# Kernel tuning notes

Measured on AMD Instinct MI355X. Metric: run time of the kernel, lower is better.

Reference implementation:

```python
import jax, jax.numpy as jnp
import numpy as np

B, N, ND = 4096, 28, 3        # batch, nodes (2 hands x 14 joints), xyz
ED, DD = 512, 256             # encoder dim, decoder dim
H, DH = 8, 64                 # heads, dim_head (inner = 512)
EDEPTH, DDEPTH = 2, 1
EMLP, DMLP = 4 * ED, 4 * DD
NM = 14                       # num_masked = int(0.5 * 28)


def _ln(x, s, b):
    m = jnp.mean(x, -1, keepdims=True)
    v = jnp.var(x, -1, keepdims=True)
    return (x - m) * jax.lax.rsqrt(v + 1e-5) * s + b


def _transformer(x, a, ln1_s, ln1_b, Wqkv, Wo, bo, ln2_s, ln2_b, W1, b1, W2, b2):
    # pre-norm transformer; adjacency a [b,n,n] enters as an additive attention bias
    b, n, _ = x.shape
    scale = DH ** -0.5
    for i in range(ln1_s.shape[0]):
        h = _ln(x, ln1_s[i], ln1_b[i])
        q, k, v = jnp.split(h @ Wqkv[i], 3, axis=-1)
        q = q.reshape(b, n, H, DH).transpose(0, 2, 1, 3)
        k = k.reshape(b, n, H, DH).transpose(0, 2, 1, 3)
        v = v.reshape(b, n, H, DH).transpose(0, 2, 1, 3)
        dots = jnp.einsum('bhid,bhjd->bhij', q, k) * scale + a[:, None]
        attn = jax.nn.softmax(dots, axis=-1)
        o = jnp.einsum('bhij,bhjd->bhid', attn, v).transpose(0, 2, 1, 3).reshape(b, n, H * DH)
        x = x + o @ Wo[i] + bo[i]
        h2 = _ln(x, ln2_s[i], ln2_b[i])
        x = x + jax.nn.gelu(h2 @ W1[i] + b1[i]) @ W2[i] + b2[i]
    return x


def setup_inputs() -> dict:
    key = jax.random.key(0)
    ks = iter(jax.random.split(key, 40))
    nrm = lambda shp, s=0.02: jax.random.normal(next(ks), shp, dtype=jnp.float32) * s
    x = jax.random.normal(next(ks), (B, N, ND), dtype=jnp.float32)
    a = jax.random.uniform(next(ks), (B, N, N), dtype=jnp.float32)
    perm = jnp.argsort(jax.random.uniform(next(ks), (B, N)), axis=-1).astype(jnp.int32)
    masked_indices, unmasked_indices = perm[:, :NM], perm[:, NM:]
    inp = dict(x=x, a=a, masked_indices=masked_indices, unmasked_indices=unmasked_indices)
    inp.update(
        W_emb=nrm((ND, ED)), b_emb=jnp.zeros((ED,), jnp.float32), pos_emb=nrm((N, ED), 0.02),
        e_ln1_s=jnp.ones((EDEPTH, ED)), e_ln1_b=jnp.zeros((EDEPTH, ED)),
        e_Wqkv=nrm((EDEPTH, ED, 3 * H * DH)), e_Wo=nrm((EDEPTH, H * DH, ED)), e_bo=jnp.zeros((EDEPTH, ED)),
        e_ln2_s=jnp.ones((EDEPTH, ED)), e_ln2_b=jnp.zeros((EDEPTH, ED)),
        e_W1=nrm((EDEPTH, ED, EMLP)), e_b1=jnp.zeros((EDEPTH, EMLP)),
        e_W2=nrm((EDEPTH, EMLP, ED)), e_b2=jnp.zeros((EDEPTH, ED)),
        enc2dec_W=nrm((ED, DD)), enc2dec_b=jnp.zeros((DD,), jnp.float32),
        mask_token=nrm((DD,), 1.0), dec_pos_emb=nrm((N, DD), 0.02),
        d_ln1_s=jnp.ones((DDEPTH, DD)), d_ln1_b=jnp.zeros((DDEPTH, DD)),
        d_Wqkv=nrm((DDEPTH, DD, 3 * H * DH)), d_Wo=nrm((DDEPTH, H * DH, DD)), d_bo=jnp.zeros((DDEPTH, DD)),
        d_ln2_s=jnp.ones((DDEPTH, DD)), d_ln2_b=jnp.zeros((DDEPTH, DD)),
        d_W1=nrm((DDEPTH, DD, DMLP)), d_b1=jnp.zeros((DDEPTH, DMLP)),
        d_W2=nrm((DDEPTH, DMLP, DD)), d_b2=jnp.zeros((DDEPTH, DD)),
        pred_W=nrm((DD, ND)), pred_b=jnp.zeros((ND,), jnp.float32),
    )
    return inp


def reference(x, a, masked_indices, unmasked_indices,
              W_emb, b_emb, pos_emb,
              e_ln1_s, e_ln1_b, e_Wqkv, e_Wo, e_bo, e_ln2_s, e_ln2_b, e_W1, e_b1, e_W2, e_b2,
              enc2dec_W, enc2dec_b, mask_token, dec_pos_emb,
              d_ln1_s, d_ln1_b, d_Wqkv, d_Wo, d_bo, d_ln2_s, d_ln2_b, d_W1, d_b1, d_W2, d_b2,
              pred_W, pred_b):
    # node embedding (1x1 conv over nodes == per-node linear) + positional embedding
    tokens = x @ W_emb + b_emb + pos_emb                                   # [B,N,ED]
    unm_tok = jnp.take_along_axis(tokens, unmasked_indices[:, :, None], axis=1)  # [B,N-NM,ED]
    masked_nodes = jnp.take_along_axis(x, masked_indices[:, :, None], axis=1)    # [B,NM,ND]
    # batched adjacency slicing (replaces the per-sample python loop in torch)
    unmasked_a = jax.vmap(lambda ai, ii: ai[ii[:, None], ii[None, :]])(a, unmasked_indices)
    enc = _transformer(unm_tok, unmasked_a,
                       e_ln1_s, e_ln1_b, e_Wqkv, e_Wo, e_bo, e_ln2_s, e_ln2_b, e_W1, e_b1, e_W2, e_b2)
    dec_tok = enc @ enc2dec_W + enc2dec_b                                  # [B,N-NM,DD]
    mask_toks = mask_token + dec_pos_emb[masked_indices]                   # [B,NM,DD]
    # NOTE: faithful to original: unmasked pos-emb tokens are computed but NOT used in the cat
    decoder_tokens = jnp.concatenate([mask_toks, dec_tok], axis=1)         # [B,N,DD]
    decoded = _transformer(decoder_tokens, a,
                           d_ln1_s, d_ln1_b, d_Wqkv, d_Wo, d_bo, d_ln2_s, d_ln2_b, d_W1, d_b1, d_W2, d_b2)
    mt = jnp.take_along_axis(decoded, masked_indices[:, :, None], axis=1)  # [B,NM,DD]
    masked_pred = mt @ pred_W + pred_b                                     # [B,NM,ND]
    recon_loss = jnp.mean((masked_pred - masked_nodes) ** 2)
    return (decoder_tokens, masked_nodes, masked_indices, masked_pred, recon_loss)
```

## Files before the change

kernel.cpp:

```cpp
#include <hip/hip_runtime.h>
#include <math.h>

#define B_TOT 4096
#define N_SEQ 28
#define NDIM 3
#define ED 512
#define DD 256
#define NH 8
#define DHD 64
#define EMLP 2048
#define DMLP 1024
#define NM 14
#define NU 14

typedef __attribute__((ext_vector_type(8))) short short8;
typedef __attribute__((ext_vector_type(4))) float f32x4;
typedef unsigned short ushort_t;
typedef unsigned int uint_t;

__device__ __forceinline__ float gelu_f(float x) {
    float t = 0.7978845608028654f * (x + 0.044715f * x * x * x);
    float e = __expf(2.0f * t);
    float th = 1.0f - 2.0f / (e + 1.0f);
    return 0.5f * x * (1.0f + th);
}
__device__ __forceinline__ ushort_t f2bf(float f) {
    union { float f; uint_t u; } c; c.f = f;
    uint_t u = c.u;
    return (ushort_t)((u + 0x7FFFu + ((u >> 16) & 1u)) >> 16);
}
__device__ __forceinline__ float bf2f(ushort_t h) {
    union { uint_t u; float f; } c; c.u = ((uint_t)h) << 16;
    return c.f;
}
__device__ __forceinline__ float bf_lo(uint_t u) {
    union { uint_t u; float f; } c; c.u = u << 16;
    return c.f;
}
__device__ __forceinline__ float bf_hi(uint_t u) {
    union { uint_t u; float f; } c; c.u = u & 0xFFFF0000u;
    return c.f;
}
__device__ __forceinline__ uint_t cvtpk(float lo, float hi) {
    uint_t r;
    asm volatile("v_cvt_pk_bf16_f32 %0, %1, %2" : "=v"(r) : "v"(lo), "v"(hi));
    return r;
}
__device__ __forceinline__ void gl_lds16(const ushort_t* g, ushort_t* l) {
    __builtin_amdgcn_global_load_lds(
        (const __attribute__((address_space(1))) unsigned int*)g,
        (__attribute__((address_space(3))) unsigned int*)l, 16, 0, 0);
}

__global__ void k_zero(float* p) { p[threadIdx.x] = 0.0f; }
__global__ void k_final(const float* acc, float* out) {
    out[0] = acc[0] * (1.0f / (float)(B_TOT * NM * NDIM));
}

__global__ void k_wconv(const float* __restrict__ W, ushort_t* __restrict__ Wt, int K, int N) {
    __shared__ float tile[32][33];
    int n0 = blockIdx.x * 32, k0 = blockIdx.y * 32;
    int tr = threadIdx.x >> 5, tc = threadIdx.x & 31;
#pragma unroll
    for (int i = 0; i < 4; ++i)
        tile[tr + i * 8][tc] = W[(size_t)(k0 + tr + i * 8) * N + n0 + tc];
    __syncthreads();
#pragma unroll
    for (int i = 0; i < 4; ++i)
        Wt[(size_t)(n0 + tr + i * 8) * K + k0 + tc] = f2bf(tile[tc][tr + i * 8]);
}

__global__ void k_embed(const float* __restrict__ x, const float* __restrict__ a,
                        const int* __restrict__ mi, const int* __restrict__ ui,
                        const float* __restrict__ W_emb, const float* __restrict__ b_emb,
                        const float* __restrict__ pos_emb,
                        ushort_t* __restrict__ X, float* __restrict__ ua,
                        float* __restrict__ out_mn, float* __restrict__ out_midx,
                        int base) {
    int s = blockIdx.x;
    int g = base + s;
    int t = threadIdx.x;
    for (int i = 0; i < NU; ++i) {
        int u = ui[g * NU + i];
        float x0 = x[((size_t)g * N_SEQ + u) * NDIM + 0];
        float x1 = x[((size_t)g * N_SEQ + u) * NDIM + 1];
        float x2 = x[((size_t)g * N_SEQ + u) * NDIM + 2];
        for (int d = t; d < ED; d += 256) {
            X[((size_t)s * NU + i) * ED + d] = f2bf(
                x0 * W_emb[d] + x1 * W_emb[ED + d] + x2 * W_emb[2 * ED + d]
                + b_emb[d] + pos_emb[(size_t)u * ED + d]);
        }
    }
    for (int idx = t; idx < NU * NU; idx += 256) {
        int i = idx / NU, j = idx % NU;
        int uii = ui[g * NU + i], ujj = ui[g * NU + j];
        ua[(size_t)s * NU * NU + idx] = a[(size_t)g * N_SEQ * N_SEQ + (size_t)uii * N_SEQ + ujj];
    }
    for (int idx = t; idx < NM * NDIM; idx += 256) {
        int i = idx / NDIM, c = idx % NDIM;
        int m = mi[g * NM + i];
        out_mn[((size_t)g * NM + i) * NDIM + c] = x[((size_t)g * N_SEQ + m) * NDIM + c];
    }
    for (int i = t; i < NM; i += 256) {
        out_midx[(size_t)g * NM + i] = (float)mi[g * NM + i];
    }
}

template <int D>
__global__ void k_ln(const ushort_t* __restrict__ in, ushort_t* __restrict__ out,
                     const float* __restrict__ sc, const float* __restrict__ bi, int M) {
    int wave = threadIdx.x >> 6;
    int lane = threadIdx.x & 63;
    int row = blockIdx.x * 4 + wave;
    if (row >= M) return;
    constexpr int PL = D / 64;
    const ushort_t* rp = in + (size_t)row * D + lane * PL;
    uint_t u[PL / 2];
    if (PL == 8) *(uint4*)u = *(const uint4*)rp;
    else *(uint2*)u = *(const uint2*)rp;
    float v[PL];
    float sum = 0.f, sq = 0.f;
#pragma unroll
    for (int q = 0; q < PL / 2; ++q) {
        v[2 * q] = bf_lo(u[q]);
        v[2 * q + 1] = bf_hi(u[q]);
    }
#pragma unroll
    for (int j = 0; j < PL; ++j) { sum += v[j]; sq += v[j] * v[j]; }
#pragma unroll
    for (int o = 32; o >= 1; o >>= 1) {
        sum += __shfl_xor(sum, o);
        sq += __shfl_xor(sq, o);
    }
    float mean = sum * (1.0f / D);
    float var = sq * (1.0f / D) - mean * mean;
    float r = rsqrtf(var + 1e-5f);
    uint_t w[PL / 2];
#pragma unroll
    for (int q = 0; q < PL / 2; ++q) {
        int d = lane * PL + 2 * q;
        float a0 = (v[2 * q] - mean) * r * sc[d] + bi[d];
        float a1 = (v[2 * q + 1] - mean) * r * sc[d + 1] + bi[d + 1];
        w[q] = (uint_t)f2bf(a0) | ((uint_t)f2bf(a1) << 16);
    }
    ushort_t* op = out + (size_t)row * D + lane * PL;
    if (PL == 8) *(uint4*)op = *(uint4*)w;
    else *(uint2*)op = *(uint2*)w;
}

template <int ACT>
__global__ __launch_bounds__(256) void k_gemm_mfma(
    const ushort_t* __restrict__ A, const ushort_t* __restrict__ Wt,
    const float* __restrict__ bias, const ushort_t* __restrict__ res,
    ushort_t* __restrict__ Cout, int M, int N, int K, int lda) {
    __shared__ __align__(16) ushort_t smem[24576];

    const int t = threadIdx.x;
    const int gx = gridDim.x;
    int flat = blockIdx.y * gx + blockIdx.x;
    int nwg = gx * gridDim.y;
    int q8 = nwg >> 3, r8 = nwg & 7;
    int xcd = flat & 7, loc = flat >> 3;
    int wg = (xcd < r8 ? xcd * (q8 + 1) : r8 * (q8 + 1) + (xcd - r8) * q8) + loc;
    const int bm = wg / gx, bn = wg % gx;

    const int lane = t & 63;
    const int wave = t >> 6;
    const int wr = wave >> 1, wc = wave & 1;
    const int l15 = lane & 15;
    const int g4 = lane >> 4;
    const int kq = (g4 ^ ((l15 >> 1) & 3)) * 8;

    const int srow = wave * 32 + (lane >> 2);
    const int scol = ((lane & 3) ^ ((lane >> 3) & 3)) * 8;
    const ushort_t* Ag = A + (size_t)(bm * 128 + srow) * lda + scol;
    const ushort_t* Bg = Wt + (size_t)(bn * 128 + srow) * K + scol;
    const int wb0 = (wave * 32) * 32;
    const int wb1 = (wave * 32 + 16) * 32;

    f32x4 acc[4][4] = {};
    const int nt = K >> 5;

#define STAGE(tile, idx)                                          \
    do {                                                          \
        int k0_ = (tile) << 5;                                    \
        ushort_t* Ab_ = smem + (idx) * 8192;                      \
        ushort_t* Bb_ = Ab_ + 4096;                               \
        gl_lds16(Ag + k0_, Ab_ + wb0);                            \
        gl_lds16(Ag + (size_t)16 * lda + k0_, Ab_ + wb1);         \
        gl_lds16(Bg + k0_, Bb_ + wb0);                            \
        gl_lds16(Bg + (size_t)16 * K + k0_, Bb_ + wb1);           \
    } while (0)

    STAGE(0, 0);
    STAGE(1, 1);

    int cur = 0;
    for (int tt = 0; tt < nt; ++tt) {
        if (tt + 1 < nt) asm volatile("s_waitcnt vmcnt(4)" ::: "memory");
        else             asm volatile("s_waitcnt vmcnt(0)" ::: "memory");
        __builtin_amdgcn_s_barrier();
        __builtin_amdgcn_sched_barrier(0);
        if (tt + 2 < nt) {
            int nidx = cur + 2; if (nidx >= 3) nidx -= 3;
            STAGE(tt + 2, nidx);
        }
        const ushort_t* Ac = smem + cur * 8192;
        const ushort_t* Bc = Ac + 4096;
        short8 af[4], bfr[4];
#pragma unroll
        for (int m = 0; m < 4; ++m)
            af[m] = *(const short8*)&Ac[(wr * 64 + m * 16 + l15) * 32 + kq];
#pragma unroll
        for (int n = 0; n < 4; ++n)
            bfr[n] = *(const short8*)&Bc[(wc * 64 + n * 16 + l15) * 32 + kq];
#pragma unroll
        for (int m = 0; m < 4; ++m)
#pragma unroll
            for (int n = 0; n < 4; ++n)
                acc[m][n] = __builtin_amdgcn_mfma_f32_16x16x32_bf16(af[m], bfr[n], acc[m][n], 0, 0, 0);
        if (++cur == 3) cur = 0;
    }
#undef STAGE

    __builtin_amdgcn_sched_barrier(0);
    __builtin_amdgcn_s_barrier();

    ushort_t* Cs = smem;
    const int erow0 = wr * 64, ecol0 = wc * 64;
#pragma unroll
    for (int m = 0; m < 4; ++m)
#pragma unroll
        for (int n = 0; n < 4; ++n)
#pragma unroll
            for (int r = 0; r < 4; ++r) {
                float v = acc[m][n][r];
                float o = __shfl_xor(v, 1);
                if (!(l15 & 1)) {
                    uint_t pk = cvtpk(v, o);
                    *(uint_t*)&Cs[(erow0 + m * 16 + g4 * 4 + r) * 136 + ecol0 + n * 16 + l15] = pk;
                }
            }
    __builtin_amdgcn_s_barrier();

    const int row = t >> 1, half = t & 1;
    const int grow = bm * 128 + row;
    const int gc0 = bn * 128 + half * 64;
    const ushort_t* rres = res ? res + (size_t)grow * N + gc0 : (const ushort_t*)0;
    ushort_t* gout = Cout + (size_t)grow * N + gc0;
#pragma unroll
    for (int c = 0; c < 8; ++c) {
        uint4 pv = *(const uint4*)&Cs[row * 136 + half * 64 + c * 8];
        uint_t* pw = (uint_t*)&pv;
        float vv[8];
#pragma unroll
        for (int q = 0; q < 4; ++q) { vv[2 * q] = bf_lo(pw[q]); vv[2 * q + 1] = bf_hi(pw[q]); }
        if (bias) {
#pragma unroll
            for (int j = 0; j < 8; ++j) vv[j] += bias[gc0 + c * 8 + j];
        }
        if (res) {
            uint4 rv = *(const uint4*)(rres + c * 8);
            uint_t* pr = (uint_t*)&rv;
#pragma unroll
            for (int q = 0; q < 4; ++q) { vv[2 * q] += bf_lo(pr[q]); vv[2 * q + 1] += bf_hi(pr[q]); }
        }
        if (ACT == 1) {
#pragma unroll
            for (int j = 0; j < 8; ++j) vv[j] = gelu_f(vv[j]);
        }
        uint4 ov;
        uint_t* po = (uint_t*)&ov;
#pragma unroll
        for (int q = 0; q < 4; ++q)
            po[q] = cvtpk(vv[2 * q], vv[2 * q + 1]);
        *(uint4*)(gout + c * 8) = ov;
    }
}

template <int NT>
__global__ __launch_bounds__(256) void k_attn_mfma(
    ushort_t* __restrict__ qkv, const float* __restrict__ bias) {
    constexpr int NTP = (NT + 15) & ~15;
    constexpr int MT = NTP / 16;
    constexpr int QS = 72;
    constexpr int VS = 40;
    __shared__ __align__(16) ushort_t smem[4 * NTP * QS * 2 + 4 * 64 * VS];
    ushort_t* Qs = smem;
    ushort_t* Ks = smem + 4 * NTP * QS;
    ushort_t* Vs = Ks + 4 * NTP * QS;
    ushort_t* Ps = smem;

    const int s = blockIdx.x, hg = blockIdx.y;
    const int t = threadIdx.x;
    const int wave = t >> 6, lane = t & 63;
    const int l15 = lane & 15, g4 = lane >> 4;

    const ushort_t* qb = qkv + (size_t)s * NT * 1536 + hg * 256;
    for (int c = t; c < 64 * NT; c += 256) {
        int c8 = c & 7;
        int rem = c >> 3;
        int r = rem % NT;
        int ph = rem / NT;
        int h = ph & 3, p = ph >> 2;
        uint4 v = *(const uint4*)(qb + (size_t)r * 1536 + p * 512 + h * 64 + c8 * 8);
        ushort_t* dst = (p ? Ks : Qs) + (h * NTP + r) * QS + c8 * 8;
        *(uint4*)dst = v;
    }
    const ushort_t* vrow = qkv + (size_t)s * NT * 1536 + 1024 + hg * 256;
    for (int c = t; c < 4 * 64 * (32 - NT); c += 256) {
        int p = c % (32 - NT);
        int hd = c / (32 - NT);
        Vs[hd * VS + NT + p] = 0;
    }
    for (int c = t; c < 4 * NT * 8; c += 256) {
        int c8 = c & 7;
        int r = (c >> 3) % NT;
        int h = (c >> 3) / NT;
        uint4 v = *(const uint4*)(vrow + (size_t)r * 1536 + h * 64 + c8 * 8);
        const uint_t* pv = (const uint_t*)&v;
#pragma unroll
        for (int j = 0; j < 4; ++j) {
            Vs[(h * 64 + c8 * 8 + 2 * j) * VS + r] = (ushort_t)(pv[j] & 0xFFFFu);
            Vs[(h * 64 + c8 * 8 + 2 * j + 1) * VS + r] = (ushort_t)(pv[j] >> 16);
        }
    }
    __syncthreads();

    const int h = wave;
    const ushort_t* Qh = Qs + h * NTP * QS;
    const ushort_t* Kh = Ks + h * NTP * QS;
    const ushort_t* Vh = Vs + h * 64 * VS;
    ushort_t* Ph = Ps + h * NTP * VS;

    f32x4 sacc[MT][MT] = {};
#pragma unroll
    for (int ks = 0; ks < 2; ++ks) {
        short8 qf[MT], kf[MT];
#pragma unroll
        for (int m = 0; m < MT; ++m)
            qf[m] = *(const short8*)&Qh[(m * 16 + l15) * QS + ks * 32 + g4 * 8];
#pragma unroll
        for (int n = 0; n < MT; ++n)
            kf[n] = *(const short8*)&Kh[(n * 16 + l15) * QS + ks * 32 + g4 * 8];
#pragma unroll
        for (int m = 0; m < MT; ++m)
#pragma unroll
            for (int n = 0; n < MT; ++n)
                sacc[m][n] = __builtin_amdgcn_mfma_f32_16x16x32_bf16(qf[m], kf[n], sacc[m][n], 0, 0, 0);
    }

    const float* bp = bias + (size_t)s * NT * NT;
    float prv[MT][MT][4];
#pragma unroll
    for (int m = 0; m < MT; ++m) {
#pragma unroll
        for (int r = 0; r < 4; ++r) {
            int i = m * 16 + g4 * 4 + r;
            float sv[MT];
#pragma unroll
            for (int n = 0; n < MT; ++n) {
                int j = n * 16 + l15;
                sv[n] = (i < NT && j < NT) ? sacc[m][n][r] * 0.125f + bp[i * NT + j] : -1e30f;
            }
            float mx = sv[0];
            if (MT > 1) mx = fmaxf(mx, sv[MT - 1]);
#pragma unroll
            for (int o = 1; o < 16; o <<= 1) mx = fmaxf(mx, __shfl_xor(mx, o));
            float sum = 0.f;
#pragma unroll
            for (int n = 0; n < MT; ++n) {
                float e = (sv[n] > -1e29f) ? __expf(sv[n] - mx) : 0.f;
                prv[m][n][r] = e;
                sum += e;
            }
#pragma unroll
            for (int o = 1; o < 16; o <<= 1) sum += __shfl_xor(sum, o);
            float rs = sum > 0.f ? 1.0f / sum : 0.f;
#pragma unroll
            for (int n = 0; n < MT; ++n) prv[m][n][r] *= rs;
        }
    }
    __syncthreads();

    if (NTP == 16) {
        for (int z = lane; z < 16 * 8; z += 64) {
            int i = z >> 3, jw = z & 7;
            *(uint_t*)&Ph[i * VS + 16 + jw * 2] = 0;
        }
    }
#pragma unroll
    for (int m = 0; m < MT; ++m)
#pragma unroll
        for (int n = 0; n < MT; ++n)
#pragma unroll
            for (int r = 0; r < 4; ++r)
                Ph[(m * 16 + g4 * 4 + r) * VS + n * 16 + l15] = f2bf(prv[m][n][r]);
    __syncthreads();

    f32x4 oacc[MT][4] = {};
    {
        short8 pf[MT], vf[4];
#pragma unroll
        for (int m = 0; m < MT; ++m)
            pf[m] = *(const short8*)&Ph[(m * 16 + l15) * VS + g4 * 8];
#pragma unroll
        for (int nd = 0; nd < 4; ++nd)
            vf[nd] = *(const short8*)&Vh[(nd * 16 + l15) * VS + g4 * 8];
#pragma unroll
        for (int m = 0; m < MT; ++m)
#pragma unroll
            for (int nd = 0; nd < 4; ++nd)
                oacc[m][nd] = __builtin_amdgcn_mfma_f32_16x16x32_bf16(pf[m], vf[nd], oacc[m][nd], 0, 0, 0);
    }

    ushort_t* Ob = qkv + (size_t)s * NT * 1536 + hg * 256 + h * 64;
#pragma unroll
    for (int m = 0; m < MT; ++m)
#pragma unroll
        for (int r = 0; r < 4; ++r) {
            int i = m * 16 + g4 * 4 + r;
            if (i < NT) {
#pragma unroll
                for (int nd = 0; nd < 4; ++nd)
                    Ob[(size_t)i * 1536 + nd * 16 + l15] = f2bf(oacc[m][nd][r]);
            }
        }
}

__global__ void k_build_dec(const ushort_t* __restrict__ dec_tok, const float* __restrict__ mask_token,
                            const float* __restrict__ dec_pos, const int* __restrict__ mi,
                            ushort_t* __restrict__ Xd, float* __restrict__ out0, int base) {
    int s = blockIdx.x;
    int g = base + s;
    int t = threadIdx.x;
    for (int idx = t; idx < N_SEQ * DD; idx += 256) {
        int i = idx / DD, d = idx % DD;
        float v;
        if (i < NM) {
            int m = mi[g * NM + i];
            v = mask_token[d] + dec_pos[(size_t)m * DD + d];
        } else {
            v = bf2f(dec_tok[((size_t)s * NU + (i - NM)) * DD + d]);
        }
        Xd[((size_t)s * N_SEQ + i) * DD + d] = f2bf(v);
        out0[((size_t)g * N_SEQ + i) * DD + d] = v;
    }
}

__global__ void k_pred(const ushort_t* __restrict__ Xd, const int* __restrict__ mi,
                       const float* __restrict__ pW, const float* __restrict__ pb,
                       const float* __restrict__ mn, float* __restrict__ out_pred,
                       float* __restrict__ loss, int base, int Bc) {
    int tid = blockIdx.x * 256 + threadIdx.x;
    int total = Bc * NM * NDIM;
    float part = 0.f;
    if (tid < total) {
        int c = tid % NDIM;
        int r = tid / NDIM;
        int i = r % NM;
        int s = r / NM;
        int g = base + s;
        int m = mi[g * NM + i];
        const ushort_t* row = Xd + ((size_t)s * N_SEQ + m) * DD;
        float acc = pb[c];
        for (int k = 0; k < DD; ++k) acc += bf2f(row[k]) * pW[k * NDIM + c];
        out_pred[((size_t)g * NM + i) * NDIM + c] = acc;
        float d = acc - mn[((size_t)g * NM + i) * NDIM + c];
        part = d * d;
    }
    __shared__ float red[256];
    red[threadIdx.x] = part;
    __syncthreads();
    for (int o = 128; o > 0; o >>= 1) {
        if (threadIdx.x < o) red[threadIdx.x] += red[threadIdx.x + o];
        __syncthreads();
    }
    if (threadIdx.x == 0) atomicAdd(loss, red[0]);
}

extern "C" void kernel_launch(void* const* d_in, const int* in_sizes, int n_in,
                              void* d_out, int out_size, void* d_ws, size_t ws_size,
                              hipStream_t stream) {
    const float* x       = (const float*)d_in[0];
    const float* a       = (const float*)d_in[1];
    const int*   mi      = (const int*)d_in[2];
    const int*   ui      = (const int*)d_in[3];
    const float* W_emb   = (const float*)d_in[4];
    const float* b_emb   = (const float*)d_in[5];
    const float* pos_emb = (const float*)d_in[6];
    const float* e_ln1_s = (const float*)d_in[7];
    const float* e_ln1_b = (const float*)d_in[8];
    const float* e_Wqkv  = (const float*)d_in[9];
    const float* e_Wo    = (const float*)d_in[10];
    const float* e_bo    = (const float*)d_in[11];
    const float* e_ln2_s = (const float*)d_in[12];
    const float* e_ln2_b = (const float*)d_in[13];
    const float* e_W1    = (const float*)d_in[14];
    const float* e_b1    = (const float*)d_in[15];
    const float* e_W2    = (const float*)d_in[16];
    const float* e_b2    = (const float*)d_in[17];
    const float* e2d_W   = (const float*)d_in[18];
    const float* e2d_b   = (const float*)d_in[19];
    const float* mask_tok= (const float*)d_in[20];
    const float* dec_pos = (const float*)d_in[21];
    const float* d_ln1_s = (const float*)d_in[22];
    const float* d_ln1_b = (const float*)d_in[23];
    const float* d_Wqkv  = (const float*)d_in[24];
    const float* d_Wo    = (const float*)d_in[25];
    const float* d_bo    = (const float*)d_in[26];
    const float* d_ln2_s = (const float*)d_in[27];
    const float* d_ln2_b = (const float*)d_in[28];
    const float* d_W1    = (const float*)d_in[29];
    const float* d_b1    = (const float*)d_in[30];
    const float* d_W2    = (const float*)d_in[31];
    const float* d_b2    = (const float*)d_in[32];
    const float* pred_W  = (const float*)d_in[33];
    const float* pred_b  = (const float*)d_in[34];

    float* out0 = (float*)d_out;
    float* out1 = out0 + (size_t)B_TOT * N_SEQ * DD;
    float* out2 = out1 + (size_t)B_TOT * NM * NDIM;
    float* out3 = out2 + (size_t)B_TOT * NM;
    float* out4 = out3 + (size_t)B_TOT * NM * NDIM;

    char* wp = (char*)d_ws;
    size_t off = 0;
    auto alloc = [&](size_t bytes) {
        size_t o = off;
        off = (off + bytes + 255) & ~(size_t)255;
        return (void*)(wp + o);
    };
    float* loss_acc = (float*)alloc(64 * 4);
    ushort_t* wt_eqkv = (ushort_t*)alloc((size_t)2 * 1536 * 512 * 2);
    ushort_t* wt_ewo  = (ushort_t*)alloc((size_t)2 * 512 * 512 * 2);
    ushort_t* wt_ew1  = (ushort_t*)alloc((size_t)2 * 2048 * 512 * 2);
    ushort_t* wt_ew2  = (ushort_t*)alloc((size_t)2 * 512 * 2048 * 2);
    ushort_t* wt_dqkv = (ushort_t*)alloc((size_t)1536 * 256 * 2);
    ushort_t* wt_dwo  = (ushort_t*)alloc((size_t)256 * 512 * 2);
    ushort_t* wt_dw1  = (ushort_t*)alloc((size_t)1024 * 256 * 2);
    ushort_t* wt_dw2  = (ushort_t*)alloc((size_t)256 * 1024 * 2);
    ushort_t* wt_e2d  = (ushort_t*)alloc((size_t)256 * 512 * 2);
    size_t fixed_bytes = off;

    const size_t per_seq = 2 * (7168 + 3584 + 7168 + 43008) + 4 * 196;
    int Bc = B_TOT;
    while (Bc > 64 && fixed_bytes + (size_t)Bc * per_seq + 8192 > ws_size) Bc >>= 1;

    ushort_t* Xbuf   = (ushort_t*)alloc((size_t)Bc * 7168 * 2);
    ushort_t* Dbuf   = (ushort_t*)alloc((size_t)Bc * 3584 * 2);
    float*    uabuf  = (float*)alloc((size_t)Bc * 196 * 4);
    ushort_t* Hbuf   = (ushort_t*)alloc((size_t)Bc * 7168 * 2);
    ushort_t* QKVbuf = (ushort_t*)alloc((size_t)Bc * 43008 * 2);

    k_zero<<<1, 64, 0, stream>>>(loss_acc);

    for (int l = 0; l < 2; ++l) {
        k_wconv<<<dim3(1536 / 32, 512 / 32), 256, 0, stream>>>(e_Wqkv + (size_t)l * 512 * 1536, wt_eqkv + (size_t)l * 1536 * 512, 512, 1536);
        k_wconv<<<dim3(512 / 32, 512 / 32), 256, 0, stream>>>(e_Wo + (size_t)l * 512 * 512, wt_ewo + (size_t)l * 512 * 512, 512, 512);
        k_wconv<<<dim3(2048 / 32, 512 / 32), 256, 0, stream>>>(e_W1 + (size_t)l * 512 * 2048, wt_ew1 + (size_t)l * 2048 * 512, 512, 2048);
        k_wconv<<<dim3(512 / 32, 2048 / 32), 256, 0, stream>>>(e_W2 + (size_t)l * 2048 * 512, wt_ew2 + (size_t)l * 512 * 2048, 2048, 512);
    }
    k_wconv<<<dim3(1536 / 32, 256 / 32), 256, 0, stream>>>(d_Wqkv, wt_dqkv, 256, 1536);
    k_wconv<<<dim3(256 / 32, 512 / 32), 256, 0, stream>>>(d_Wo, wt_dwo, 512, 256);
    k_wconv<<<dim3(1024 / 32, 256 / 32), 256, 0, stream>>>(d_W1, wt_dw1, 256, 1024);
    k_wconv<<<dim3(256 / 32, 1024 / 32), 256, 0, stream>>>(d_W2, wt_dw2, 1024, 256);
    k_wconv<<<dim3(256 / 32, 512 / 32), 256, 0, stream>>>(e2d_W, wt_e2d, 512, 256);

    const int nchunk = B_TOT / Bc;
    for (int c = 0; c < nchunk; ++c) {
        int base = c * Bc;
        int M = Bc * NU;
        int Md = Bc * N_SEQ;

        k_embed<<<Bc, 256, 0, stream>>>(x, a, mi, ui, W_emb, b_emb, pos_emb,
                                        Xbuf, uabuf, out1, out2, base);
        for (int l = 0; l < 2; ++l) {
            k_ln<ED><<<M / 4, 256, 0, stream>>>(Xbuf, Hbuf, e_ln1_s + l * ED, e_ln1_b + l * ED, M);
            k_gemm_mfma<0><<<dim3(1536 / 128, M / 128), 256, 0, stream>>>(
                Hbuf, wt_eqkv + (size_t)l * 1536 * 512, nullptr, nullptr, QKVbuf, M, 1536, ED, ED);
            k_attn_mfma<NU><<<dim3(Bc, 2), 256, 0, stream>>>(QKVbuf, uabuf);
            k_gemm_mfma<0><<<dim3(ED / 128, M / 128), 256, 0, stream>>>(
                QKVbuf, wt_ewo + (size_t)l * 512 * 512, e_bo + l * ED, Xbuf, Xbuf, M, ED, 512, 1536);
            k_ln<ED><<<M / 4, 256, 0, stream>>>(Xbuf, Hbuf, e_ln2_s + l * ED, e_ln2_b + l * ED, M);
            k_gemm_mfma<1><<<dim3(EMLP / 128, M / 128), 256, 0, stream>>>(
                Hbuf, wt_ew1 + (size_t)l * 2048 * 512, e_b1 + l * EMLP, nullptr, QKVbuf, M, EMLP, ED, ED);
            k_gemm_mfma<0><<<dim3(ED / 128, M / 128), 256, 0, stream>>>(
                QKVbuf, wt_ew2 + (size_t)l * 512 * 2048, e_b2 + l * ED, Xbuf, Xbuf, M, ED, EMLP, EMLP);
        }
        k_gemm_mfma<0><<<dim3(DD / 128, M / 128), 256, 0, stream>>>(
            Xbuf, wt_e2d, e2d_b, nullptr, Dbuf, M, DD, ED, ED);
        k_build_dec<<<Bc, 256, 0, stream>>>(Dbuf, mask_tok, dec_pos, mi, Xbuf, out0, base);
        k_ln<DD><<<Md / 4, 256, 0, stream>>>(Xbuf, Hbuf, d_ln1_s, d_ln1_b, Md);
        k_gemm_mfma<0><<<dim3(1536 / 128, Md / 128), 256, 0, stream>>>(
            Hbuf, wt_dqkv, nullptr, nullptr, QKVbuf, Md, 1536, DD, DD);
        k_attn_mfma<N_SEQ><<<dim3(Bc, 2), 256, 0, stream>>>(QKVbuf, a + (size_t)base * N_SEQ * N_SEQ);
        k_gemm_mfma<0><<<dim3(DD / 128, Md / 128), 256, 0, stream>>>(
            QKVbuf, wt_dwo, d_bo, Xbuf, Xbuf, Md, DD, 512, 1536);
        k_ln<DD><<<Md / 4, 256, 0, stream>>>(Xbuf, Hbuf, d_ln2_s, d_ln2_b, Md);
        k_gemm_mfma<1><<<dim3(DMLP / 128, Md / 128), 256, 0, stream>>>(
            Hbuf, wt_dw1, d_b1, nullptr, QKVbuf, Md, DMLP, DD, DD);
        k_gemm_mfma<0><<<dim3(DD / 128, Md / 128), 256, 0, stream>>>(
            QKVbuf, wt_dw2, d_b2, Xbuf, Xbuf, Md, DD, DMLP, DMLP);
        int tot = Bc * NM * NDIM;
        k_pred<<<(tot + 255) / 256, 256, 0, stream>>>(
            Xbuf, mi, pred_W, pred_b, out1, out3, loss_acc, base, Bc);
    }
    k_final<<<1, 1, 0, stream>>>(loss_acc, out4);
}
```

Baseline: 2.651 ms.

## Give each wave private double-buffered LDS tiles to drop per-iteration block barrier

The GEMM kernel now has each wave stage its own 64-row A and B slices into a private LDS region with double buffering, instead of sharing a block-wide triple buffer. This removes the s_barrier in the k-loop, replacing it with a local lgkmcnt wait before the next prefetch. In exchange, every A and B slice is loaded twice by different waves, which doubles global and LDS fill traffic, and LDS usage rises to 64 KB per block, which may cut occupancy.

```diff
diff --git a/kernel.cpp b/kernel.cpp
--- a/kernel.cpp
+++ b/kernel.cpp
@@ -153,7 +153,7 @@
     const ushort_t* __restrict__ A, const ushort_t* __restrict__ Wt,
     const float* __restrict__ bias, const ushort_t* __restrict__ res,
     ushort_t* __restrict__ Cout, int M, int N, int K, int lda) {
-    __shared__ __align__(16) ushort_t smem[24576];
+    __shared__ __align__(16) ushort_t smem[32768];
 
     const int t = threadIdx.x;
     const int gx = gridDim.x;
@@ -171,25 +171,27 @@
     const int g4 = lane >> 4;
     const int kq = (g4 ^ ((l15 >> 1) & 3)) * 8;
 
-    const int srow = wave * 32 + (lane >> 2);
     const int scol = ((lane & 3) ^ ((lane >> 3) & 3)) * 8;
-    const ushort_t* Ag = A + (size_t)(bm * 128 + srow) * lda + scol;
-    const ushort_t* Bg = Wt + (size_t)(bn * 128 + srow) * K + scol;
-    const int wb0 = (wave * 32) * 32;
-    const int wb1 = (wave * 32 + 16) * 32;
+    const ushort_t* Ag = A + (size_t)(bm * 128 + wr * 64 + (lane >> 2)) * lda + scol;
+    const ushort_t* Bg = Wt + (size_t)(bn * 128 + wc * 64 + (lane >> 2)) * K + scol;
+    ushort_t* wbase = smem + wave * 8192;
+    const ushort_t* Ard = wbase + l15 * 32 + kq;
 
     f32x4 acc[4][4] = {};
     const int nt = K >> 5;
 
-#define STAGE(tile, idx)                                          \
+#define STAGE(tile, b)                                            \
     do {                                                          \
         int k0_ = (tile) << 5;                                    \
-        ushort_t* Ab_ = smem + (idx) * 8192;                      \
-        ushort_t* Bb_ = Ab_ + 4096;                               \
-        gl_lds16(Ag + k0_, Ab_ + wb0);                            \
-        gl_lds16(Ag + (size_t)16 * lda + k0_, Ab_ + wb1);         \
-        gl_lds16(Bg + k0_, Bb_ + wb0);                            \
-        gl_lds16(Bg + (size_t)16 * K + k0_, Bb_ + wb1);           \
+        ushort_t* Ab_ = wbase + (b) * 4096;                       \
+        gl_lds16(Ag + k0_, Ab_);                                  \
+        gl_lds16(Ag + (size_t)16 * lda + k0_, Ab_ + 512);         \
+        gl_lds16(Ag + (size_t)32 * lda + k0_, Ab_ + 1024);        \
+        gl_lds16(Ag + (size_t)48 * lda + k0_, Ab_ + 1536);        \
+        gl_lds16(Bg + k0_, Ab_ + 2048);                           \
+        gl_lds16(Bg + (size_t)16 * K + k0_, Ab_ + 2560);          \
+        gl_lds16(Bg + (size_t)32 * K + k0_, Ab_ + 3072);          \
+        gl_lds16(Bg + (size_t)48 * K + k0_, Ab_ + 3584);          \
     } while (0)
 
     STAGE(0, 0);
@@ -197,29 +199,26 @@
 
     int cur = 0;
     for (int tt = 0; tt < nt; ++tt) {
-        if (tt + 1 < nt) asm volatile("s_waitcnt vmcnt(4)" ::: "memory");
+        if (tt + 1 < nt) asm volatile("s_waitcnt vmcnt(8)" ::: "memory");
         else             asm volatile("s_waitcnt vmcnt(0)" ::: "memory");
-        __builtin_amdgcn_s_barrier();
         __builtin_amdgcn_sched_barrier(0);
-        if (tt + 2 < nt) {
-            int nidx = cur + 2; if (nidx >= 3) nidx -= 3;
-            STAGE(tt + 2, nidx);
-        }
-        const ushort_t* Ac = smem + cur * 8192;
-        const ushort_t* Bc = Ac + 4096;
+        const ushort_t* Ac = Ard + cur * 4096;
         short8 af[4], bfr[4];
 #pragma unroll
         for (int m = 0; m < 4; ++m)
-            af[m] = *(const short8*)&Ac[(wr * 64 + m * 16 + l15) * 32 + kq];
+            af[m] = *(const short8*)(Ac + m * 512);
 #pragma unroll
         for (int n = 0; n < 4; ++n)
-            bfr[n] = *(const short8*)&Bc[(wc * 64 + n * 16 + l15) * 32 + kq];
+            bfr[n] = *(const short8*)(Ac + 2048 + n * 512);
+        asm volatile("s_waitcnt lgkmcnt(0)" ::: "memory");
+        __builtin_amdgcn_sched_barrier(0);
+        if (tt + 2 < nt) STAGE(tt + 2, cur);
 #pragma unroll
         for (int m = 0; m < 4; ++m)
 #pragma unroll
             for (int n = 0; n < 4; ++n)
                 acc[m][n] = __builtin_amdgcn_mfma_f32_16x16x32_bf16(af[m], bfr[n], acc[m][n], 0, 0, 0);
-        if (++cur == 3) cur = 0;
+        cur ^= 1;
     }
 #undef STAGE
 
```

New measurement: 3.114 ms. 17.5% more time.
